# Kernel optimization log

Measured on AMD Instinct MI355X. Metric: run time of the kernel, lower is better.

Reference implementation:

```python
import jax, jax.numpy as jnp
import numpy as np

W_RNN = 768
DEC_H = 256
TAGS = 2
TAG_EM = 32


def setup_inputs() -> dict:
    key = jax.random.key(0)
    ks = jax.random.split(key, 8)
    B, T = 64, 512
    in_size = W_RNN + TAG_EM  # 800
    aff_in = W_RNN + DEC_H    # 1024
    sents_vec = jax.random.normal(ks[0], (B, T, W_RNN), dtype=jnp.float32)
    mask_cls = jnp.ones((B, T), dtype=jnp.float32)
    # xavier-uniform-ish init for weights, zeros for biases (matches param_init)
    def xavier(k, shape):
        fan_in, fan_out = shape[1], shape[0]
        lim = float(np.sqrt(6.0 / (fan_in + fan_out)))
        return jax.random.uniform(k, shape, jnp.float32, -lim, lim)
    Wih = xavier(ks[1], (4 * DEC_H, in_size))
    Whh = xavier(ks[2], (4 * DEC_H, DEC_H))
    bih = jnp.zeros((4 * DEC_H,), jnp.float32)
    bhh = jnp.zeros((4 * DEC_H,), jnp.float32)
    Waff = xavier(ks[3], (TAGS, aff_in))
    baff = jnp.zeros((TAGS,), jnp.float32)
    tag_em = xavier(ks[4], (TAGS, TAG_EM))
    return {"sents_vec": sents_vec, "mask_cls": mask_cls, "Wih": Wih,
            "Whh": Whh, "bih": bih, "bhh": bhh, "Waff": Waff,
            "baff": baff, "tag_em": tag_em}


def reference(sents_vec, mask_cls, Wih, Whh, bih, bhh, Waff, baff, tag_em):
    # Dropout is treated in eval mode (identity), as is standard for a
    # deterministic correctness baseline.
    B, T, D = sents_vec.shape
    H = DEC_H
    h0 = jnp.zeros((B, H), sents_vec.dtype)
    go = jnp.zeros((B, TAG_EM), sents_vec.dtype)

    Hs = jnp.swapaxes(sents_vec, 0, 1)        # [T, B, D]
    Ms = jnp.swapaxes(mask_cls, 0, 1)[..., None]  # [T, B, 1]

    def step(carry, xs):
        h, c, yem = carry
        Hi, mi = xs
        x = jnp.concatenate([yem, Hi], axis=1)            # [B, 800]
        gates = x @ Wih.T + h @ Whh.T + (bih + bhh)       # [B, 4H]
        i_g, f_g, g_g, o_g = jnp.split(gates, 4, axis=1)  # torch LSTMCell order
        c_new = jax.nn.sigmoid(f_g) * c + jax.nn.sigmoid(i_g) * jnp.tanh(g_g)
        h_new = jax.nn.sigmoid(o_g) * jnp.tanh(c_new)
        score = jnp.concatenate([h_new, Hi], axis=1) @ Waff.T + baff  # [B, TAGS]
        pred = jnp.argmax(score, axis=-1)                 # [B]
        yem_new = tag_em[pred]                            # [B, TAG_EM]
        h_out = h_new * mi + h * (1.0 - mi)
        c_out = c_new * mi + c * (1.0 - mi)
        return (h_out, c_out, yem_new), score

    _, scores = jax.lax.scan(step, (h0, h0, go), (Hs, Ms))  # [T, B, TAGS]
    scores = jnp.swapaxes(scores, 0, 1)                      # [B, T, TAGS]
    return jax.nn.log_softmax(scores, axis=2)
```

## Files before the change

### kernel.cpp

```cpp
#include <hip/hip_runtime.h>
#include <cstdint>
#include <cstddef>

#define TT 512
#define BB 64
#define HH 256
#define NG 1024
#define DI 768
#define KY 32

#define LDP 56

typedef __attribute__((ext_vector_type(8))) short bfrag_t;
typedef __attribute__((ext_vector_type(4))) float f4_t;

__device__ __forceinline__ float sigf(float x) {
    return __fdividef(1.f, 1.f + __expf(-x));
}
__device__ __forceinline__ float tanhfast(float x) {
    return fmaf(2.f, sigf(2.f * x), -1.f);
}
__device__ __forceinline__ unsigned short bf_hi(float x) {
    return (unsigned short)(__float_as_uint(x) >> 16);
}
__device__ __forceinline__ float bf_hi_f(float x) {
    return __uint_as_float(__float_as_uint(x) & 0xffff0000u);
}

__global__ __launch_bounds__(256) void kgemm2(
    const float* __restrict__ sents, const float* __restrict__ Wih,
    const float* __restrict__ bih, const float* __restrict__ bhh,
    float* __restrict__ gpre, int t0)
{
    __shared__ unsigned short Ah[128 * LDP], Al[128 * LDP];
    __shared__ unsigned short Bh[128 * LDP], Bl[128 * LDP];

    const int tid = threadIdx.x;
    const int nb = blockIdx.x;
    const int mb = blockIdx.y;
    const int wv = tid >> 6, lane = tid & 63;
    const int wm = (wv >> 1) * 64, wn = (wv & 1) * 64;
    const int fl = lane & 15, quad = lane >> 4;

    f4_t acc[4][4];
#pragma unroll
    for (int mi = 0; mi < 4; ++mi)
#pragma unroll
        for (int ni = 0; ni < 4; ++ni) acc[mi][ni] = (f4_t)0.f;

    const int sr = tid >> 1, sk = (tid & 1) * 16;
    const int gr = mb * 128 + sr;
    const float* aptr = sents + ((size_t)(gr & 63) * TT + t0 + (gr >> 6)) * DI + sk;
    const float* bptr = Wih + (size_t)(nb * 128 + sr) * 800 + KY + sk;

    for (int k0 = 0; k0 < DI; k0 += 32) {
        float4 av[4], bv[4];
#pragma unroll
        for (int i = 0; i < 4; ++i) {
            av[i] = *(const float4*)(aptr + k0 + i * 4);
            bv[i] = *(const float4*)(bptr + k0 + i * 4);
        }
        __syncthreads();
#pragma unroll
        for (int i = 0; i < 4; ++i) {
            ushort4 h4, l4;
            h4.x = bf_hi(av[i].x); l4.x = bf_hi(av[i].x - bf_hi_f(av[i].x));
            h4.y = bf_hi(av[i].y); l4.y = bf_hi(av[i].y - bf_hi_f(av[i].y));
            h4.z = bf_hi(av[i].z); l4.z = bf_hi(av[i].z - bf_hi_f(av[i].z));
            h4.w = bf_hi(av[i].w); l4.w = bf_hi(av[i].w - bf_hi_f(av[i].w));
            *(ushort4*)&Ah[sr * LDP + sk + i * 4] = h4;
            *(ushort4*)&Al[sr * LDP + sk + i * 4] = l4;
            h4.x = bf_hi(bv[i].x); l4.x = bf_hi(bv[i].x - bf_hi_f(bv[i].x));
            h4.y = bf_hi(bv[i].y); l4.y = bf_hi(bv[i].y - bf_hi_f(bv[i].y));
            h4.z = bf_hi(bv[i].z); l4.z = bf_hi(bv[i].z - bf_hi_f(bv[i].z));
            h4.w = bf_hi(bv[i].w); l4.w = bf_hi(bv[i].w - bf_hi_f(bv[i].w));
            *(ushort4*)&Bh[sr * LDP + sk + i * 4] = h4;
            *(ushort4*)&Bl[sr * LDP + sk + i * 4] = l4;
        }
        __syncthreads();

        bfrag_t ah[4], al2[4], bh[4], bl2[4];
#pragma unroll
        for (int mi = 0; mi < 4; ++mi) {
            int row = wm + mi * 16 + fl;
            ah[mi]  = *(const bfrag_t*)&Ah[row * LDP + quad * 8];
            al2[mi] = *(const bfrag_t*)&Al[row * LDP + quad * 8];
        }
#pragma unroll
        for (int ni = 0; ni < 4; ++ni) {
            int col = wn + ni * 16 + fl;
            bh[ni]  = *(const bfrag_t*)&Bh[col * LDP + quad * 8];
            bl2[ni] = *(const bfrag_t*)&Bl[col * LDP + quad * 8];
        }
#pragma unroll
        for (int mi = 0; mi < 4; ++mi)
#pragma unroll
            for (int ni = 0; ni < 4; ++ni) {
                acc[mi][ni] = __builtin_amdgcn_mfma_f32_16x16x32_bf16(
                    ah[mi], bh[ni], acc[mi][ni], 0, 0, 0);
                acc[mi][ni] = __builtin_amdgcn_mfma_f32_16x16x32_bf16(
                    ah[mi], bl2[ni], acc[mi][ni], 0, 0, 0);
                acc[mi][ni] = __builtin_amdgcn_mfma_f32_16x16x32_bf16(
                    al2[mi], bh[ni], acc[mi][ni], 0, 0, 0);
            }
    }

#pragma unroll
    for (int ni = 0; ni < 4; ++ni) {
        int gcol = nb * 128 + wn + ni * 16 + fl;
        float bias = bih[gcol] + bhh[gcol];
#pragma unroll
        for (int mi = 0; mi < 4; ++mi) {
            int grow = mb * 128 + wm + mi * 16 + quad * 4;
#pragma unroll
            for (int r = 0; r < 4; ++r)
                gpre[(size_t)(grow + r) * NG + gcol] = acc[mi][ni][r] + bias;
        }
    }
}

__global__ __launch_bounds__(256) void kshi(
    const float* __restrict__ sents, const float* __restrict__ Waff,
    const float* __restrict__ baff, float* __restrict__ shi, int t0)
{
    const int tid = threadIdx.x;
    const int lane = tid & 63;
    const int r = blockIdx.x * 4 + (tid >> 6);
    const int b = r & 63, tl = r >> 6;
    const float* hi = sents + ((size_t)b * TT + t0 + tl) * DI;
    float p0 = 0.f, p1 = 0.f;
#pragma unroll
    for (int kk = 0; kk < 12; ++kk) {
        int k = kk * 64 + lane;
        float x = hi[k];
        p0 = fmaf(x, Waff[HH + k], p0);
        p1 = fmaf(x, Waff[NG + HH + k], p1);
    }
#pragma unroll
    for (int off = 32; off >= 1; off >>= 1) {
        p0 += __shfl_xor(p0, off, 64);
        p1 += __shfl_xor(p1, off, 64);
    }
    if (lane == 0) {
        shi[(size_t)r * 2 + 0] = p0 + baff[0];
        shi[(size_t)r * 2 + 1] = p1 + baff[1];
    }
}

__global__ void kinit(unsigned long long* __restrict__ hbox) {
    hbox[(size_t)blockIdx.x * 512 + threadIdx.x] = 0ull;
}

__global__ __launch_bounds__(512, 1) void krec3(
    const float* __restrict__ gpre,
    const float* __restrict__ shi,
    const float* __restrict__ Whh,
    const float* __restrict__ mask,
    float* __restrict__ out,
    float* __restrict__ sh, float* __restrict__ sc, int* __restrict__ sp,
    unsigned long long* __restrict__ hbox,
    const float* __restrict__ Wih, const float* __restrict__ tag,
    const float* __restrict__ Waff,
    int t0, int Tc, int first)
{
    const int blk = blockIdx.x;
    const int g = blk >> 6, b = blk & 63;
    const int tid = threadIdx.x;
    const int w = tid >> 6, lane = tid & 63;
    const int jl = lane & 7, kq = lane >> 3;
    const int jh = w * 8 + jl;
    const int jglob = g * 64 + jh;

    __shared__ float hk[8 * 36];
    __shared__ float hnS[HH];
    __shared__ float P[2][4][64];
    __shared__ float tg[2][KY];
    __shared__ float red[8][2];

    float4 wreg[4][8];
#pragma unroll
    for (int gt = 0; gt < 4; ++gt) {
        const float4* src = (const float4*)(Whh + (size_t)(gt * HH + jglob) * HH + kq * 32);
#pragma unroll
        for (int kk = 0; kk < 8; ++kk) wreg[gt][kk] = src[kk];
    }

    const int sdim = w * 32 + (lane & 31);
    const int stag = lane >> 5;
    const float waffR = Waff[(size_t)stag * NG + sdim];

    if (tid < 2 * KY) tg[tid >> 5][tid & 31] = tag[tid];
    __syncthreads();
    {
        int r = tid >> 8, rem = tid & 255, gt = rem >> 6, j2 = rem & 63;
        int row = gt * HH + g * 64 + j2;
        const float4* wr = (const float4*)(Wih + (size_t)row * 800);
        float s = 0.f;
#pragma unroll
        for (int kk = 0; kk < 8; ++kk) {
            float4 v = wr[kk];
            s = fmaf(v.x, tg[r][kk * 4 + 0], s);
            s = fmaf(v.y, tg[r][kk * 4 + 1], s);
            s = fmaf(v.z, tg[r][kk * 4 + 2], s);
            s = fmaf(v.w, tg[r][kk * 4 + 3], s);
        }
        P[r][gt][j2] = s;
    }

    float creg; int pred;
    if (first) {
        creg = 0.f; pred = -1;
        if (tid < 72) ((float4*)hk)[tid] = make_float4(0.f, 0.f, 0.f, 0.f);
    } else {
        creg = sc[(size_t)b * HH + jglob];
        pred = sp[b];
        if (tid < HH) hk[(tid >> 5) * 36 + (tid & 31)] = sh[(size_t)b * HH + tid];
    }
    __syncthreads();

    float cgp0, cgp1, cgp2, cgp3, cmi, cs0, cs1;
    {
        const float* gp = gpre + ((size_t)0 * BB + b) * NG;
        cgp0 = gp[0 * HH + jglob]; cgp1 = gp[1 * HH + jglob];
        cgp2 = gp[2 * HH + jglob]; cgp3 = gp[3 * HH + jglob];
        cmi = mask[(size_t)b * TT + t0];
        const float* s2 = shi + ((size_t)0 * BB + b) * 2;
        cs0 = s2[0]; cs1 = s2[1];
    }

    for (int tl = 0; tl < Tc; ++tl) {
        const int t = t0 + tl;
        const int p = t & 1;

        float pv0 = 0.f, pv1 = 0.f, pv2 = 0.f, pv3 = 0.f;
        if (pred >= 0) {
            pv0 = P[pred][0][jh]; pv1 = P[pred][1][jh];
            pv2 = P[pred][2][jh]; pv3 = P[pred][3][jh];
        }

        float a0 = 0.f, a1 = 0.f, a2 = 0.f, a3 = 0.f;
        const float4* h4 = (const float4*)(hk + kq * 36);
#pragma unroll
        for (int kk = 0; kk < 8; ++kk) {
            float4 hv = h4[kk];
            a0 = fmaf(wreg[0][kk].x, hv.x, a0); a0 = fmaf(wreg[0][kk].y, hv.y, a0);
            a0 = fmaf(wreg[0][kk].z, hv.z, a0); a0 = fmaf(wreg[0][kk].w, hv.w, a0);
            a1 = fmaf(wreg[1][kk].x, hv.x, a1); a1 = fmaf(wreg[1][kk].y, hv.y, a1);
            a1 = fmaf(wreg[1][kk].z, hv.z, a1); a1 = fmaf(wreg[1][kk].w, hv.w, a1);
            a2 = fmaf(wreg[2][kk].x, hv.x, a2); a2 = fmaf(wreg[2][kk].y, hv.y, a2);
            a2 = fmaf(wreg[2][kk].z, hv.z, a2); a2 = fmaf(wreg[2][kk].w, hv.w, a2);
            a3 = fmaf(wreg[3][kk].x, hv.x, a3); a3 = fmaf(wreg[3][kk].y, hv.y, a3);
            a3 = fmaf(wreg[3][kk].z, hv.z, a3); a3 = fmaf(wreg[3][kk].w, hv.w, a3);
        }
        a0 += __shfl_xor(a0, 8, 64); a0 += __shfl_xor(a0, 16, 64); a0 += __shfl_xor(a0, 32, 64);
        a1 += __shfl_xor(a1, 8, 64); a1 += __shfl_xor(a1, 16, 64); a1 += __shfl_xor(a1, 32, 64);
        a2 += __shfl_xor(a2, 8, 64); a2 += __shfl_xor(a2, 16, 64); a2 += __shfl_xor(a2, 32, 64);
        a3 += __shfl_xor(a3, 8, 64); a3 += __shfl_xor(a3, 16, 64); a3 += __shfl_xor(a3, 32, 64);

        float gi = a0 + cgp0 + pv0;
        float gf = a1 + cgp1 + pv1;
        float gg = a2 + cgp2 + pv2;
        float go = a3 + cgp3 + pv3;
        float ig = sigf(gi), fg = sigf(gf);
        float g2 = tanhfast(gg), og = sigf(go);
        float cn = fmaf(fg, creg, ig * g2);
        float hn = og * tanhfast(cn);
        float mi = cmi;
        float s2v0 = cs0, s2v1 = cs1;
        creg = cn * mi + creg * (1.f - mi);

        if (kq == 0) {
            unsigned long long wd =
                ((unsigned long long)__float_as_uint(hn) << 32) | (unsigned)(t + 1);
            __hip_atomic_store(&hbox[((size_t)(p * BB + b) * 4 + g) * 64 + jh], wd,
                               __ATOMIC_RELAXED, __HIP_MEMORY_SCOPE_AGENT);
            hnS[jglob] = hn;
        }

        if (tl + 1 < Tc) {
            const float* gp2 = gpre + ((size_t)(tl + 1) * BB + b) * NG;
            cgp0 = gp2[0 * HH + jglob]; cgp1 = gp2[1 * HH + jglob];
            cgp2 = gp2[2 * HH + jglob]; cgp3 = gp2[3 * HH + jglob];
            cmi = mask[(size_t)b * TT + t + 1];
            const float* s2n = shi + ((size_t)(tl + 1) * BB + b) * 2;
            cs0 = s2n[0]; cs1 = s2n[1];
        }

        if (tid < 192) {
            int pg = (g + 1 + (tid >> 6)) & 3, j2 = tid & 63;
            const unsigned long long* wp = &hbox[((size_t)(p * BB + b) * 4 + pg) * 64 + j2];
            unsigned long long wv;
            do {
                wv = __hip_atomic_load(wp, __ATOMIC_RELAXED, __HIP_MEMORY_SCOPE_AGENT);
            } while ((unsigned)wv != (unsigned)(t + 1));
            hnS[pg * 64 + j2] = __uint_as_float((unsigned)(wv >> 32));
        }
        __syncthreads();

        if (tid < HH) {
            int idx = (tid >> 5) * 36 + (tid & 31);
            float hold = hk[idx];
            hk[idx] = hnS[tid] * mi + hold * (1.f - mi);
        }
        float prod = hnS[sdim] * waffR;
        prod += __shfl_xor(prod, 1, 64);
        prod += __shfl_xor(prod, 2, 64);
        prod += __shfl_xor(prod, 4, 64);
        prod += __shfl_xor(prod, 8, 64);
        prod += __shfl_xor(prod, 16, 64);
        if ((lane & 31) == 0) red[w][stag] = prod;
        __syncthreads();

        float s0 = red[0][0];
        s0 += red[1][0]; s0 += red[2][0]; s0 += red[3][0];
        s0 += red[4][0]; s0 += red[5][0]; s0 += red[6][0]; s0 += red[7][0];
        float s1 = red[0][1];
        s1 += red[1][1]; s1 += red[2][1]; s1 += red[3][1];
        s1 += red[4][1]; s1 += red[5][1]; s1 += red[6][1]; s1 += red[7][1];
        float ts0 = s0 + s2v0, ts1 = s1 + s2v1;
        pred = (ts1 > ts0) ? 1 : 0;
        if (g == 0 && tid == 0) {
            float m = fmaxf(ts0, ts1);
            float lse = m + log1pf(expf(-fabsf(ts0 - ts1)));
            float* op = out + ((size_t)b * TT + t) * 2;
            op[0] = ts0 - lse; op[1] = ts1 - lse;
        }
    }

    if (kq == 0) {
        sh[(size_t)b * HH + jglob] = hk[(jglob >> 5) * 36 + (jglob & 31)];
        sc[(size_t)b * HH + jglob] = creg;
    }
    if (g == 0 && tid == 0) sp[b] = pred;
}

extern "C" void kernel_launch(void* const* d_in, const int* in_sizes, int n_in,
                              void* d_out, int out_size, void* d_ws, size_t ws_size,
                              hipStream_t stream) {
    (void)in_sizes; (void)n_in; (void)out_size;
    const float* sents = (const float*)d_in[0];
    const float* mask  = (const float*)d_in[1];
    const float* Wih   = (const float*)d_in[2];
    const float* Whh   = (const float*)d_in[3];
    const float* bih   = (const float*)d_in[4];
    const float* bhh   = (const float*)d_in[5];
    const float* Waff  = (const float*)d_in[6];
    const float* baff  = (const float*)d_in[7];
    const float* tag   = (const float*)d_in[8];
    float* out = (float*)d_out;

    const size_t fixed = (size_t)BB * HH * 4 * 2
                       + BB * 4
                       + (size_t)2 * BB * 4 * 64 * 8
                       + 4096;
    int Tc = 8;
    const int cands[7] = {512, 256, 128, 64, 32, 16, 8};
    for (int i = 0; i < 7; ++i) {
        size_t need = (size_t)cands[i] * BB * NG * 4
                    + (size_t)cands[i] * BB * 2 * 4
                    + fixed;
        if (need <= ws_size) { Tc = cands[i]; break; }
    }

    char* wsp = (char*)d_ws;
    float* gpre = (float*)wsp; wsp += (size_t)Tc * BB * NG * 4;
    float* shiw = (float*)wsp; wsp += (size_t)Tc * BB * 2 * 4;
    float* shst = (float*)wsp; wsp += (size_t)BB * HH * 4;
    float* scst = (float*)wsp; wsp += (size_t)BB * HH * 4;
    int*   spst = (int*)wsp;   wsp += BB * 4;
    unsigned long long* hbox = (unsigned long long*)wsp;

    kinit<<<dim3(64), 512, 0, stream>>>(hbox);

    const int nch = TT / Tc;
    for (int c = 0; c < nch; ++c) {
        const int t0 = c * Tc;
        kgemm2<<<dim3(8, Tc * 64 / 128), 256, 0, stream>>>(sents, Wih, bih, bhh, gpre, t0);
        kshi<<<dim3(Tc * 16), 256, 0, stream>>>(sents, Waff, baff, shiw, t0);
        krec3<<<dim3(256), 512, 0, stream>>>(gpre, shiw, Whh, mask, out,
                                             shst, scst, spst, hbox,
                                             Wih, tag, Waff, t0, Tc, (c == 0) ? 1 : 0);
    }
}
```

Before: 1.289 ms.

## Fuse input-projection GEMM into persistent recurrent kernel with producer warps

```diff
diff --git a/kernel.cpp b/kernel.cpp
--- a/kernel.cpp
+++ b/kernel.cpp
@@ -9,7 +9,9 @@
 #define DI 768
 #define KY 32
 
-#define LDP 56
+#define PA 776
+#define PR 276
+#define NW 32
 
 typedef __attribute__((ext_vector_type(8))) short bfrag_t;
 typedef __attribute__((ext_vector_type(4))) float f4_t;
@@ -27,171 +29,152 @@
     return __uint_as_float(__float_as_uint(x) & 0xffff0000u);
 }
 
-__global__ __launch_bounds__(256) void kgemm2(
-    const float* __restrict__ sents, const float* __restrict__ Wih,
-    const float* __restrict__ bih, const float* __restrict__ bhh,
-    float* __restrict__ gpre, int t0)
+__global__ __launch_bounds__(256) void kprew(
+    const float* __restrict__ Wih, const float* __restrict__ Waff,
+    unsigned short* __restrict__ Bsh, unsigned short* __restrict__ Bsl)
 {
-    __shared__ unsigned short Ah[128 * LDP], Al[128 * LDP];
-    __shared__ unsigned short Bh[128 * LDP], Bl[128 * LDP];
-
-    const int tid = threadIdx.x;
-    const int nb = blockIdx.x;
-    const int mb = blockIdx.y;
-    const int wv = tid >> 6, lane = tid & 63;
-    const int wm = (wv >> 1) * 64, wn = (wv & 1) * 64;
-    const int fl = lane & 15, quad = lane >> 4;
-
-    f4_t acc[4][4];
-#pragma unroll
-    for (int mi = 0; mi < 4; ++mi)
-#pragma unroll
-        for (int ni = 0; ni < 4; ++ni) acc[mi][ni] = (f4_t)0.f;
-
-    const int sr = tid >> 1, sk = (tid & 1) * 16;
-    const int gr = mb * 128 + sr;
-    const float* aptr = sents + ((size_t)(gr & 63) * TT + t0 + (gr >> 6)) * DI + sk;
-    const float* bptr = Wih + (size_t)(nb * 128 + sr) * 800 + KY + sk;
-
-    for (int k0 = 0; k0 < DI; k0 += 32) {
-        float4 av[4], bv[4];
-#pragma unroll
-        for (int i = 0; i < 4; ++i) {
-            av[i] = *(const float4*)(aptr + k0 + i * 4);
-            bv[i] = *(const float4*)(bptr + k0 + i * 4);
-        }
-        __syncthreads();
-#pragma unroll
-        for (int i = 0; i < 4; ++i) {
-            ushort4 h4, l4;
-            h4.x = bf_hi(av[i].x); l4.x = bf_hi(av[i].x - bf_hi_f(av[i].x));
-            h4.y = bf_hi(av[i].y); l4.y = bf_hi(av[i].y - bf_hi_f(av[i].y));
-            h4.z = bf_hi(av[i].z); l4.z = bf_hi(av[i].z - bf_hi_f(av[i].z));
-            h4.w = bf_hi(av[i].w); l4.w = bf_hi(av[i].w - bf_hi_f(av[i].w));
-            *(ushort4*)&Ah[sr * LDP + sk + i * 4] = h4;
-            *(ushort4*)&Al[sr * LDP + sk + i * 4] = l4;
-            h4.x = bf_hi(bv[i].x); l4.x = bf_hi(bv[i].x - bf_hi_f(bv[i].x));
-            h4.y = bf_hi(bv[i].y); l4.y = bf_hi(bv[i].y - bf_hi_f(bv[i].y));
-            h4.z = bf_hi(bv[i].z); l4.z = bf_hi(bv[i].z - bf_hi_f(bv[i].z));
-            h4.w = bf_hi(bv[i].w); l4.w = bf_hi(bv[i].w - bf_hi_f(bv[i].w));
-            *(ushort4*)&Bh[sr * LDP + sk + i * 4] = h4;
-            *(ushort4*)&Bl[sr * LDP + sk + i * 4] = l4;
-        }
-        __syncthreads();
-
-        bfrag_t ah[4], al2[4], bh[4], bl2[4];
-#pragma unroll
-        for (int mi = 0; mi < 4; ++mi) {
-            int row = wm + mi * 16 + fl;
-            ah[mi]  = *(const bfrag_t*)&Ah[row * LDP + quad * 8];
-            al2[mi] = *(const bfrag_t*)&Al[row * LDP + quad * 8];
-        }
-#pragma unroll
-        for (int ni = 0; ni < 4; ++ni) {
-            int col = wn + ni * 16 + fl;
-            bh[ni]  = *(const bfrag_t*)&Bh[col * LDP + quad * 8];
-            bl2[ni] = *(const bfrag_t*)&Bl[col * LDP + quad * 8];
-        }
-#pragma unroll
-        for (int mi = 0; mi < 4; ++mi)
-#pragma unroll
-            for (int ni = 0; ni < 4; ++ni) {
-                acc[mi][ni] = __builtin_amdgcn_mfma_f32_16x16x32_bf16(
-                    ah[mi], bh[ni], acc[mi][ni], 0, 0, 0);
-                acc[mi][ni] = __builtin_amdgcn_mfma_f32_16x16x32_bf16(
-                    ah[mi], bl2[ni], acc[mi][ni], 0, 0, 0);
-                acc[mi][ni] = __builtin_amdgcn_mfma_f32_16x16x32_bf16(
-                    al2[mi], bh[ni], acc[mi][ni], 0, 0, 0);
-            }
-    }
-
-#pragma unroll
-    for (int ni = 0; ni < 4; ++ni) {
-        int gcol = nb * 128 + wn + ni * 16 + fl;
-        float bias = bih[gcol] + bhh[gcol];
-#pragma unroll
-        for (int mi = 0; mi < 4; ++mi) {
-            int grow = mb * 128 + wm + mi * 16 + quad * 4;
-#pragma unroll
-            for (int r = 0; r < 4; ++r)
-                gpre[(size_t)(grow + r) * NG + gcol] = acc[mi][ni][r] + bias;
-        }
-    }
-}
-
-__global__ __launch_bounds__(256) void kshi(
-    const float* __restrict__ sents, const float* __restrict__ Waff,
-    const float* __restrict__ baff, float* __restrict__ shi, int t0)
-{
-    const int tid = threadIdx.x;
-    const int lane = tid & 63;
-    const int r = blockIdx.x * 4 + (tid >> 6);
-    const int b = r & 63, tl = r >> 6;
-    const float* hi = sents + ((size_t)b * TT + t0 + tl) * DI;
-    float p0 = 0.f, p1 = 0.f;
-#pragma unroll
-    for (int kk = 0; kk < 12; ++kk) {
-        int k = kk * 64 + lane;
-        float x = hi[k];
-        p0 = fmaf(x, Waff[HH + k], p0);
-        p1 = fmaf(x, Waff[NG + HH + k], p1);
-    }
-#pragma unroll
-    for (int off = 32; off >= 1; off >>= 1) {
-        p0 += __shfl_xor(p0, off, 64);
-        p1 += __shfl_xor(p1, off, 64);
-    }
-    if (lane == 0) {
-        shi[(size_t)r * 2 + 0] = p0 + baff[0];
-        shi[(size_t)r * 2 + 1] = p1 + baff[1];
-    }
+    const int base = (blockIdx.x * 256 + threadIdx.x) * 4;
+    const int row = base / 768;
+    const int k = base % 768;
+    float4 v;
+    if (row < 1024)      v = *(const float4*)(Wih + (size_t)row * 800 + KY + k);
+    else if (row < 1026) v = *(const float4*)(Waff + (size_t)(row - 1024) * NG + HH + k);
+    else                 v = make_float4(0.f, 0.f, 0.f, 0.f);
+    ushort4 h4, l4;
+    h4.x = bf_hi(v.x); l4.x = bf_hi(v.x - bf_hi_f(v.x));
+    h4.y = bf_hi(v.y); l4.y = bf_hi(v.y - bf_hi_f(v.y));
+    h4.z = bf_hi(v.z); l4.z = bf_hi(v.z - bf_hi_f(v.z));
+    h4.w = bf_hi(v.w); l4.w = bf_hi(v.w - bf_hi_f(v.w));
+    *(ushort4*)&Bsh[base] = h4;
+    *(ushort4*)&Bsl[base] = l4;
 }
 
 __global__ void kinit(unsigned long long* __restrict__ hbox) {
     hbox[(size_t)blockIdx.x * 512 + threadIdx.x] = 0ull;
 }
 
-__global__ __launch_bounds__(512, 1) void krec3(
-    const float* __restrict__ gpre,
-    const float* __restrict__ shi,
+
+#define GEMM_KSTEP(_pb, _k0) do {                                                        \
+    const int _ao = gfl * PA + (_k0) + gquad * 8;                                        \
+    bfrag_t _ahf = *(const bfrag_t*)&Ah[_pb][_ao];                                       \
+    bfrag_t _alf = *(const bfrag_t*)&Al[_pb][_ao];                                       \
+    _Pragma("unroll")                                                                    \
+    for (int _ni = 0; _ni < 4; ++_ni) {                                                  \
+        const size_t _bo = (size_t)(wgi * 256 + g * 64 + _ni * 16 + gfl) * 768           \
+                         + (_k0) + gquad * 8;                                            \
+        bfrag_t _bhf = *(const bfrag_t*)&Bsh[_bo];                                       \
+        bfrag_t _blf = *(const bfrag_t*)&Bsl[_bo];                                       \
+        acc[_ni] = __builtin_amdgcn_mfma_f32_16x16x32_bf16(_ahf, _bhf, acc[_ni], 0,0,0); \
+        acc[_ni] = __builtin_amdgcn_mfma_f32_16x16x32_bf16(_ahf, _blf, acc[_ni], 0,0,0); \
+        acc[_ni] = __builtin_amdgcn_mfma_f32_16x16x32_bf16(_alf, _bhf, acc[_ni], 0,0,0); \
+    }                                                                                    \
+    if (wgi == 0) {                                                                      \
+        const size_t _bo = (size_t)(1024 + gfl) * 768 + (_k0) + gquad * 8;               \
+        bfrag_t _bhf = *(const bfrag_t*)&Bsh[_bo];                                       \
+        bfrag_t _blf = *(const bfrag_t*)&Bsl[_bo];                                       \
+        acc[4] = __builtin_amdgcn_mfma_f32_16x16x32_bf16(_ahf, _bhf, acc[4], 0,0,0);     \
+        acc[4] = __builtin_amdgcn_mfma_f32_16x16x32_bf16(_ahf, _blf, acc[4], 0,0,0);     \
+        acc[4] = __builtin_amdgcn_mfma_f32_16x16x32_bf16(_alf, _bhf, acc[4], 0,0,0);     \
+    }                                                                                    \
+} while (0)
+
+#define STAGE_A(_pb2, _tbase) do {                                                       \
+    const int _r = gtid >> 4, _c = gtid & 15;                                            \
+    const float* _as = sents + ((size_t)b * TT + (_tbase) + _r) * DI + _c * 48;          \
+    _Pragma("unroll")                                                                    \
+    for (int _i = 0; _i < 12; ++_i) {                                                    \
+        float4 _v = *(const float4*)(_as + _i * 4);                                      \
+        ushort4 _h4, _l4;                                                                \
+        _h4.x = bf_hi(_v.x); _l4.x = bf_hi(_v.x - bf_hi_f(_v.x));                        \
+        _h4.y = bf_hi(_v.y); _l4.y = bf_hi(_v.y - bf_hi_f(_v.y));                        \
+        _h4.z = bf_hi(_v.z); _l4.z = bf_hi(_v.z - bf_hi_f(_v.z));                        \
+        _h4.w = bf_hi(_v.w); _l4.w = bf_hi(_v.w - bf_hi_f(_v.w));                        \
+        *(ushort4*)&Ah[_pb2][_r * PA + _c * 48 + _i * 4] = _h4;                          \
+        *(ushort4*)&Al[_pb2][_r * PA + _c * 48 + _i * 4] = _l4;                          \
+    }                                                                                    \
+} while (0)
+
+#define RING_EPI(_rs2) do {                                                              \
+    _Pragma("unroll")                                                                    \
+    for (int _ni = 0; _ni < 4; ++_ni)                                                    \
+        _Pragma("unroll")                                                                \
+        for (int _r2 = 0; _r2 < 4; ++_r2)                                                \
+            ring[_rs2][(gquad * 4 + _r2) * PR + wgi * 64 + _ni * 16 + gfl] = acc[_ni][_r2]; \
+    if (wgi == 0) {                                                                      \
+        _Pragma("unroll")                                                                \
+        for (int _r2 = 0; _r2 < 4; ++_r2)                                                \
+            ring[_rs2][(gquad * 4 + _r2) * PR + 256 + gfl] = acc[4][_r2];                \
+    }                                                                                    \
+    _Pragma("unroll")                                                                    \
+    for (int _i = 0; _i < 5; ++_i) acc[_i] = (f4_t)0.f;                                  \
+} while (0)
+
+__global__ __launch_bounds__(768, 3) void krecg(
+    const float* __restrict__ sents,
+    const unsigned short* __restrict__ Bsh,
+    const unsigned short* __restrict__ Bsl,
     const float* __restrict__ Whh,
     const float* __restrict__ mask,
+    const float* __restrict__ bih, const float* __restrict__ bhh,
+    const float* __restrict__ baff,
     float* __restrict__ out,
-    float* __restrict__ sh, float* __restrict__ sc, int* __restrict__ sp,
     unsigned long long* __restrict__ hbox,
     const float* __restrict__ Wih, const float* __restrict__ tag,
-    const float* __restrict__ Waff,
-    int t0, int Tc, int first)
+    const float* __restrict__ Waff)
 {
     const int blk = blockIdx.x;
     const int g = blk >> 6, b = blk & 63;
     const int tid = threadIdx.x;
-    const int w = tid >> 6, lane = tid & 63;
-    const int jl = lane & 7, kq = lane >> 3;
-    const int jh = w * 8 + jl;
-    const int jglob = g * 64 + jh;
-
+
+    __shared__ unsigned short Ah[2][16 * PA];
+    __shared__ unsigned short Al[2][16 * PA];
+    __shared__ float ring[2][16 * PR];
     __shared__ float hk[8 * 36];
     __shared__ float hnS[HH];
     __shared__ float P[2][4][64];
     __shared__ float tg[2][KY];
     __shared__ float red[8][2];
 
-    float4 wreg[4][8];
-#pragma unroll
-    for (int gt = 0; gt < 4; ++gt) {
-        const float4* src = (const float4*)(Whh + (size_t)(gt * HH + jglob) * HH + kq * 32);
-#pragma unroll
-        for (int kk = 0; kk < 8; ++kk) wreg[gt][kk] = src[kk];
-    }
-
+    const int w = tid >> 6, lane = tid & 63;
+    const int jl = lane & 7, kq = lane >> 3;
+    const int jh = w * 8 + jl;
+    const int jglob = g * 64 + jh;
     const int sdim = w * 32 + (lane & 31);
     const int stag = lane >> 5;
-    const float waffR = Waff[(size_t)stag * NG + sdim];
+    const int gtid = tid - 512;
+    const int wgi = (gtid >> 6) & 3, glane = gtid & 63;
+    const int gfl = glane & 15, gquad = glane >> 4;
+
+    f4_t acc[5];
+#pragma unroll
+    for (int i = 0; i < 5; ++i) acc[i] = (f4_t)0.f;
+
+    float4 wreg[4][8];
+    float bia0 = 0.f, bia1 = 0.f, bia2 = 0.f, bia3 = 0.f;
+    float bf0v = 0.f, bf1v = 0.f, waffR = 0.f, cmi = 0.f, creg = 0.f;
+    int pred = -1;
+    if (tid < 512) {
+#pragma unroll
+        for (int gt = 0; gt < 4; ++gt) {
+            const float4* src = (const float4*)(Whh + (size_t)(gt * HH + jglob) * HH + kq * 32);
+#pragma unroll
+            for (int kk = 0; kk < 8; ++kk) wreg[gt][kk] = src[kk];
+        }
+        bia0 = bih[0 * HH + jglob] + bhh[0 * HH + jglob];
+        bia1 = bih[1 * HH + jglob] + bhh[1 * HH + jglob];
+        bia2 = bih[2 * HH + jglob] + bhh[2 * HH + jglob];
+        bia3 = bih[3 * HH + jglob] + bhh[3 * HH + jglob];
+        bf0v = baff[0]; bf1v = baff[1];
+        waffR = Waff[(size_t)stag * NG + sdim];
+        cmi = mask[(size_t)b * TT];
+    }
 
     if (tid < 2 * KY) tg[tid >> 5][tid & 31] = tag[tid];
+    if (tid < 72) ((float4*)hk)[tid] = make_float4(0.f, 0.f, 0.f, 0.f);
+    if (tid >= 512) STAGE_A(0, 0);
     __syncthreads();
-    {
+
+    if (tid < 512) {
         int r = tid >> 8, rem = tid & 255, gt = rem >> 6, j2 = rem & 63;
         int row = gt * HH + g * 64 + j2;
         const float4* wr = (const float4*)(Wih + (size_t)row * 800);
@@ -205,139 +188,134 @@
             s = fmaf(v.w, tg[r][kk * 4 + 3], s);
         }
         P[r][gt][j2] = s;
-    }
-
-    float creg; int pred;
-    if (first) {
-        creg = 0.f; pred = -1;
-        if (tid < 72) ((float4*)hk)[tid] = make_float4(0.f, 0.f, 0.f, 0.f);
     } else {
-        creg = sc[(size_t)b * HH + jglob];
-        pred = sp[b];
-        if (tid < HH) hk[(tid >> 5) * 36 + (tid & 31)] = sh[(size_t)b * HH + tid];
+        for (int ks = 0; ks < 24; ++ks) GEMM_KSTEP(0, ks * 32);
+        RING_EPI(0);
+        STAGE_A(1, 16);
     }
     __syncthreads();
 
-    float cgp0, cgp1, cgp2, cgp3, cmi, cs0, cs1;
-    {
-        const float* gp = gpre + ((size_t)0 * BB + b) * NG;
-        cgp0 = gp[0 * HH + jglob]; cgp1 = gp[1 * HH + jglob];
-        cgp2 = gp[2 * HH + jglob]; cgp3 = gp[3 * HH + jglob];
-        cmi = mask[(size_t)b * TT + t0];
-        const float* s2 = shi + ((size_t)0 * BB + b) * 2;
-        cs0 = s2[0]; cs1 = s2[1];
+    for (int s = 0; s < TT; ++s) {
+        const int W = s >> 4, ws = s & 15, p = s & 1, rs = W & 1;
+        float mi = 0.f, s2v0 = 0.f, s2v1 = 0.f;
+
+        if (tid < 512) {
+            float pv0 = 0.f, pv1 = 0.f, pv2 = 0.f, pv3 = 0.f;
+            if (pred >= 0) {
+                pv0 = P[pred][0][jh]; pv1 = P[pred][1][jh];
+                pv2 = P[pred][2][jh]; pv3 = P[pred][3][jh];
+            }
+            const int rb = ws * PR;
+            const float ga0 = ring[rs][rb + jh] + bia0;
+            const float ga1 = ring[rs][rb + 64 + jh] + bia1;
+            const float ga2 = ring[rs][rb + 128 + jh] + bia2;
+            const float ga3 = ring[rs][rb + 192 + jh] + bia3;
+            s2v0 = ring[rs][rb + 256] + bf0v;
+            s2v1 = ring[rs][rb + 257] + bf1v;
+
+            float a0 = 0.f, a1 = 0.f, a2 = 0.f, a3 = 0.f;
+            const float4* h4 = (const float4*)(hk + kq * 36);
+#pragma unroll
+            for (int kk = 0; kk < 8; ++kk) {
+                float4 hv = h4[kk];
+                a0 = fmaf(wreg[0][kk].x, hv.x, a0); a0 = fmaf(wreg[0][kk].y, hv.y, a0);
+                a0 = fmaf(wreg[0][kk].z, hv.z, a0); a0 = fmaf(wreg[0][kk].w, hv.w, a0);
+                a1 = fmaf(wreg[1][kk].x, hv.x, a1); a1 = fmaf(wreg[1][kk].y, hv.y, a1);
+                a1 = fmaf(wreg[1][kk].z, hv.z, a1); a1 = fmaf(wreg[1][kk].w, hv.w, a1);
+                a2 = fmaf(wreg[2][kk].x, hv.x, a2); a2 = fmaf(wreg[2][kk].y, hv.y, a2);
+                a2 = fmaf(wreg[2][kk].z, hv.z, a2); a2 = fmaf(wreg[2][kk].w, hv.w, a2);
+                a3 = fmaf(wreg[3][kk].x, hv.x, a3); a3 = fmaf(wreg[3][kk].y, hv.y, a3);
+                a3 = fmaf(wreg[3][kk].z, hv.z, a3); a3 = fmaf(wreg[3][kk].w, hv.w, a3);
+            }
+            a0 += __shfl_xor(a0, 8, 64); a0 += __shfl_xor(a0, 16, 64); a0 += __shfl_xor(a0, 32, 64);
+            a1 += __shfl_xor(a1, 8, 64); a1 += __shfl_xor(a1, 16, 64); a1 += __shfl_xor(a1, 32, 64);
+            a2 += __shfl_xor(a2, 8, 64); a2 += __shfl_xor(a2, 16, 64); a2 += __shfl_xor(a2, 32, 64);
+            a3 += __shfl_xor(a3, 8, 64); a3 += __shfl_xor(a3, 16, 64); a3 += __shfl_xor(a3, 32, 64);
+
+            float gi = a0 + ga0 + pv0;
+            float gf = a1 + ga1 + pv1;
+            float gg = a2 + ga2 + pv2;
+            float go = a3 + ga3 + pv3;
+            float ig = sigf(gi), fg = sigf(gf);
+            float g2 = tanhfast(gg), og = sigf(go);
+            float cn = fmaf(fg, creg, ig * g2);
+            float hn = og * tanhfast(cn);
+            mi = cmi;
+            creg = cn * mi + creg * (1.f - mi);
+
+            if (kq == 0) {
+                unsigned long long wd =
+                    ((unsigned long long)__float_as_uint(hn) << 32) | (unsigned)(s + 1);
+                __hip_atomic_store(&hbox[((size_t)(p * BB + b) * 4 + g) * 64 + jh], wd,
+                                   __ATOMIC_RELAXED, __HIP_MEMORY_SCOPE_AGENT);
+                hnS[jglob] = hn;
+            }
+            if (s + 1 < TT) cmi = mask[(size_t)b * TT + s + 1];
+
+            if (tid < 192) {
+                int pg = (g + 1 + (tid >> 6)) & 3, j2 = tid & 63;
+                const unsigned long long* wp = &hbox[((size_t)(p * BB + b) * 4 + pg) * 64 + j2];
+                unsigned long long wv;
+                do {
+                    wv = __hip_atomic_load(wp, __ATOMIC_RELAXED, __HIP_MEMORY_SCOPE_AGENT);
+                } while ((unsigned)wv != (unsigned)(s + 1));
+                hnS[pg * 64 + j2] = __uint_as_float((unsigned)(wv >> 32));
+            }
+        } else {
+            const int Wn = W + 1;
+            if (Wn < NW) {
+                const int pb = Wn & 1;
+                if (ws < 12) {
+                    GEMM_KSTEP(pb, ws * 64);
+                    GEMM_KSTEP(pb, ws * 64 + 32);
+                } else if (ws == 12) {
+                    if (W + 2 < NW) STAGE_A((W + 2) & 1, (W + 2) * 16);
+                } else if (ws == 15) {
+                    RING_EPI(pb);
+                }
+            }
+        }
+        __syncthreads();
+
+        if (tid < 512) {
+            if (tid < HH) {
+                int idx = (tid >> 5) * 36 + (tid & 31);
+                float hold = hk[idx];
+                hk[idx] = hnS[tid] * mi + hold * (1.f - mi);
+            }
+            float prod = hnS[sdim] * waffR;
+            prod += __shfl_xor(prod, 1, 64);
+            prod += __shfl_xor(prod, 2, 64);
+            prod += __shfl_xor(prod, 4, 64);
+            prod += __shfl_xor(prod, 8, 64);
+            prod += __shfl_xor(prod, 16, 64);
+            if ((lane & 31) == 0) red[w][stag] = prod;
+        }
+        __syncthreads();
+
+        if (tid < 512) {
+            float s0 = red[0][0];
+            s0 += red[1][0]; s0 += red[2][0]; s0 += red[3][0];
+            s0 += red[4][0]; s0 += red[5][0]; s0 += red[6][0]; s0 += red[7][0];
+            float s1 = red[0][1];
+            s1 += red[1][1]; s1 += red[2][1]; s1 += red[3][1];
+            s1 += red[4][1]; s1 += red[5][1]; s1 += red[6][1]; s1 += red[7][1];
+            float ts0 = s0 + s2v0, ts1 = s1 + s2v1;
+            pred = (ts1 > ts0) ? 1 : 0;
+            if (g == 0 && tid == 0) {
+                float m = fmaxf(ts0, ts1);
+                float lse = m + log1pf(expf(-fabsf(ts0 - ts1)));
+                float* op = out + ((size_t)b * TT + s) * 2;
+                op[0] = ts0 - lse; op[1] = ts1 - lse;
+            }
+        }
     }
-
-    for (int tl = 0; tl < Tc; ++tl) {
-        const int t = t0 + tl;
-        const int p = t & 1;
-
-        float pv0 = 0.f, pv1 = 0.f, pv2 = 0.f, pv3 = 0.f;
-        if (pred >= 0) {
-            pv0 = P[pred][0][jh]; pv1 = P[pred][1][jh];
-            pv2 = P[pred][2][jh]; pv3 = P[pred][3][jh];
-        }
-
-        float a0 = 0.f, a1 = 0.f, a2 = 0.f, a3 = 0.f;
-        const float4* h4 = (const float4*)(hk + kq * 36);
-#pragma unroll
-        for (int kk = 0; kk < 8; ++kk) {
-            float4 hv = h4[kk];
-            a0 = fmaf(wreg[0][kk].x, hv.x, a0); a0 = fmaf(wreg[0][kk].y, hv.y, a0);
-            a0 = fmaf(wreg[0][kk].z, hv.z, a0); a0 = fmaf(wreg[0][kk].w, hv.w, a0);
-            a1 = fmaf(wreg[1][kk].x, hv.x, a1); a1 = fmaf(wreg[1][kk].y, hv.y, a1);
-            a1 = fmaf(wreg[1][kk].z, hv.z, a1); a1 = fmaf(wreg[1][kk].w, hv.w, a1);
-            a2 = fmaf(wreg[2][kk].x, hv.x, a2); a2 = fmaf(wreg[2][kk].y, hv.y, a2);
-            a2 = fmaf(wreg[2][kk].z, hv.z, a2); a2 = fmaf(wreg[2][kk].w, hv.w, a2);
-            a3 = fmaf(wreg[3][kk].x, hv.x, a3); a3 = fmaf(wreg[3][kk].y, hv.y, a3);
-            a3 = fmaf(wreg[3][kk].z, hv.z, a3); a3 = fmaf(wreg[3][kk].w, hv.w, a3);
-        }
-        a0 += __shfl_xor(a0, 8, 64); a0 += __shfl_xor(a0, 16, 64); a0 += __shfl_xor(a0, 32, 64);
-        a1 += __shfl_xor(a1, 8, 64); a1 += __shfl_xor(a1, 16, 64); a1 += __shfl_xor(a1, 32, 64);
-        a2 += __shfl_xor(a2, 8, 64); a2 += __shfl_xor(a2, 16, 64); a2 += __shfl_xor(a2, 32, 64);
-        a3 += __shfl_xor(a3, 8, 64); a3 += __shfl_xor(a3, 16, 64); a3 += __shfl_xor(a3, 32, 64);
-
-        float gi = a0 + cgp0 + pv0;
-        float gf = a1 + cgp1 + pv1;
-        float gg = a2 + cgp2 + pv2;
-        float go = a3 + cgp3 + pv3;
-        float ig = sigf(gi), fg = sigf(gf);
-        float g2 = tanhfast(gg), og = sigf(go);
-        float cn = fmaf(fg, creg, ig * g2);
-        float hn = og * tanhfast(cn);
-        float mi = cmi;
-        float s2v0 = cs0, s2v1 = cs1;
-        creg = cn * mi + creg * (1.f - mi);
-
-        if (kq == 0) {
-            unsigned long long wd =
-                ((unsigned long long)__float_as_uint(hn) << 32) | (unsigned)(t + 1);
-            __hip_atomic_store(&hbox[((size_t)(p * BB + b) * 4 + g) * 64 + jh], wd,
-                               __ATOMIC_RELAXED, __HIP_MEMORY_SCOPE_AGENT);
-            hnS[jglob] = hn;
-        }
-
-        if (tl + 1 < Tc) {
-            const float* gp2 = gpre + ((size_t)(tl + 1) * BB + b) * NG;
-            cgp0 = gp2[0 * HH + jglob]; cgp1 = gp2[1 * HH + jglob];
-            cgp2 = gp2[2 * HH + jglob]; cgp3 = gp2[3 * HH + jglob];
-            cmi = mask[(size_t)b * TT + t + 1];
-            const float* s2n = shi + ((size_t)(tl + 1) * BB + b) * 2;
-            cs0 = s2n[0]; cs1 = s2n[1];
-        }
-
-        if (tid < 192) {
-            int pg = (g + 1 + (tid >> 6)) & 3, j2 = tid & 63;
-            const unsigned long long* wp = &hbox[((size_t)(p * BB + b) * 4 + pg) * 64 + j2];
-            unsigned long long wv;
-            do {
-                wv = __hip_atomic_load(wp, __ATOMIC_RELAXED, __HIP_MEMORY_SCOPE_AGENT);
-            } while ((unsigned)wv != (unsigned)(t + 1));
-            hnS[pg * 64 + j2] = __uint_as_float((unsigned)(wv >> 32));
-        }
-        __syncthreads();
-
-        if (tid < HH) {
-            int idx = (tid >> 5) * 36 + (tid & 31);
-            float hold = hk[idx];
-            hk[idx] = hnS[tid] * mi + hold * (1.f - mi);
-        }
-        float prod = hnS[sdim] * waffR;
-        prod += __shfl_xor(prod, 1, 64);
-        prod += __shfl_xor(prod, 2, 64);
-        prod += __shfl_xor(prod, 4, 64);
-        prod += __shfl_xor(prod, 8, 64);
-        prod += __shfl_xor(prod, 16, 64);
-        if ((lane & 31) == 0) red[w][stag] = prod;
-        __syncthreads();
-
-        float s0 = red[0][0];
-        s0 += red[1][0]; s0 += red[2][0]; s0 += red[3][0];
-        s0 += red[4][0]; s0 += red[5][0]; s0 += red[6][0]; s0 += red[7][0];
-        float s1 = red[0][1];
-        s1 += red[1][1]; s1 += red[2][1]; s1 += red[3][1];
-        s1 += red[4][1]; s1 += red[5][1]; s1 += red[6][1]; s1 += red[7][1];
-        float ts0 = s0 + s2v0, ts1 = s1 + s2v1;
-        pred = (ts1 > ts0) ? 1 : 0;
-        if (g == 0 && tid == 0) {
-            float m = fmaxf(ts0, ts1);
-            float lse = m + log1pf(expf(-fabsf(ts0 - ts1)));
-            float* op = out + ((size_t)b * TT + t) * 2;
-            op[0] = ts0 - lse; op[1] = ts1 - lse;
-        }
-    }
-
-    if (kq == 0) {
-        sh[(size_t)b * HH + jglob] = hk[(jglob >> 5) * 36 + (jglob & 31)];
-        sc[(size_t)b * HH + jglob] = creg;
-    }
-    if (g == 0 && tid == 0) sp[b] = pred;
 }
 
 extern "C" void kernel_launch(void* const* d_in, const int* in_sizes, int n_in,
                               void* d_out, int out_size, void* d_ws, size_t ws_size,
                               hipStream_t stream) {
-    (void)in_sizes; (void)n_in; (void)out_size;
+    (void)in_sizes; (void)n_in; (void)out_size; (void)ws_size;
     const float* sents = (const float*)d_in[0];
     const float* mask  = (const float*)d_in[1];
     const float* Wih   = (const float*)d_in[2];
@@ -349,36 +327,14 @@
     const float* tag   = (const float*)d_in[8];
     float* out = (float*)d_out;
 
-    const size_t fixed = (size_t)BB * HH * 4 * 2
-                       + BB * 4
-                       + (size_t)2 * BB * 4 * 64 * 8
-                       + 4096;
-    int Tc = 8;
-    const int cands[7] = {512, 256, 128, 64, 32, 16, 8};
-    for (int i = 0; i < 7; ++i) {
-        size_t need = (size_t)cands[i] * BB * NG * 4
-                    + (size_t)cands[i] * BB * 2 * 4
-                    + fixed;
-        if (need <= ws_size) { Tc = cands[i]; break; }
-    }
-
     char* wsp = (char*)d_ws;
-    float* gpre = (float*)wsp; wsp += (size_t)Tc * BB * NG * 4;
-    float* shiw = (float*)wsp; wsp += (size_t)Tc * BB * 2 * 4;
-    float* shst = (float*)wsp; wsp += (size_t)BB * HH * 4;
-    float* scst = (float*)wsp; wsp += (size_t)BB * HH * 4;
-    int*   spst = (int*)wsp;   wsp += BB * 4;
-    unsigned long long* hbox = (unsigned long long*)wsp;
+    unsigned short* Bsh = (unsigned short*)wsp; wsp += (size_t)1040 * 768 * 2;
+    unsigned short* Bsl = (unsigned short*)wsp; wsp += (size_t)1040 * 768 * 2;
+    uintptr_t up = ((uintptr_t)wsp + 7) & ~(uintptr_t)7;
+    unsigned long long* hbox = (unsigned long long*)up;
 
     kinit<<<dim3(64), 512, 0, stream>>>(hbox);
-
-    const int nch = TT / Tc;
-    for (int c = 0; c < nch; ++c) {
-        const int t0 = c * Tc;
-        kgemm2<<<dim3(8, Tc * 64 / 128), 256, 0, stream>>>(sents, Wih, bih, bhh, gpre, t0);
-        kshi<<<dim3(Tc * 16), 256, 0, stream>>>(sents, Waff, baff, shiw, t0);
-        krec3<<<dim3(256), 512, 0, stream>>>(gpre, shiw, Whh, mask, out,
-                                             shst, scst, spst, hbox,
-                                             Wih, tag, Waff, t0, Tc, (c == 0) ? 1 : 0);
-    }
-}
+    kprew<<<dim3(780), 256, 0, stream>>>(Wih, Waff, Bsh, Bsl);
+    krecg<<<dim3(256), 768, 0, stream>>>(sents, Bsh, Bsl, Whh, mask, bih, bhh,
+                                         baff, out, hbox, Wih, tag, Waff);
+}
```

After: 3.668 ms. 185% more time.
